# Optimization experiments

Hardware: AMD Instinct MI355X
Metric: run time of the kernel (lower is better)

The kernel has to match this reference:

```python
import jax, jax.numpy as jnp
import numpy as np

# Canonical topology: root object with K arrays, each array has L number leaves.
# Weights are tied across paths (tie_weights_containers=tie_weights_primitives=True),
# NumberEmbedder runs in eval mode with initial buffers mean=0, sqmean=1 -> identity norm.

K, L, D = 8192, 128, 64


def setup_inputs() -> dict:
    key = jax.random.key(0)
    ks = jax.random.split(key, 16)
    s = 1.0 / np.sqrt(D)
    return {
        "x": jax.random.normal(ks[0], (K, L), dtype=jnp.float32),
        "W_num": jax.random.normal(ks[1], (D, 1), dtype=jnp.float32) * s,
        "b_num": jax.random.normal(ks[2], (D,), dtype=jnp.float32) * s,
        "W_ih": jax.random.normal(ks[3], (4 * D, 2 * D), dtype=jnp.float32) * s,
        "W_hh": jax.random.normal(ks[4], (4 * D, D), dtype=jnp.float32) * s,
        "b_ih": jax.random.normal(ks[5], (4 * D,), dtype=jnp.float32) * s,
        "b_hh": jax.random.normal(ks[6], (4 * D,), dtype=jnp.float32) * s,
        "W_aout": jax.random.normal(ks[7], (D, D), dtype=jnp.float32) * s,
        "b_aout": jax.random.normal(ks[8], (D,), dtype=jnp.float32) * s,
        "W_fh": jax.random.normal(ks[9], (D, D), dtype=jnp.float32) * s,
        "b_fh": jax.random.normal(ks[10], (D,), dtype=jnp.float32) * s,
        "W_iouh": jax.random.normal(ks[11], (3 * D, D), dtype=jnp.float32) * s,
        "b_iouh": jax.random.normal(ks[12], (3 * D,), dtype=jnp.float32) * s,
        "W_oout": jax.random.normal(ks[13], (D, D), dtype=jnp.float32) * s,
        "b_oout": jax.random.normal(ks[14], (D,), dtype=jnp.float32) * s,
    }


def _forward(x, W_num, b_num, W_ih, W_hh, b_ih, b_hh, W_aout, b_aout,
             W_fh, b_fh, W_iouh, b_iouh, W_oout, b_oout):
    d = W_hh.shape[1]
    # --- NumberEmbedder: Linear(1, d) on identity-normalized numbers; c = 0 ---
    emb = x[..., None] * W_num[:, 0] + b_num          # [K, L, d]
    xs = jnp.transpose(emb, (1, 0, 2))                # [L, K, d] time-major for scan
    # --- ArrayEmbedder: LSTMCell over children; input = cat(child_h, child_c) ---
    # child_c is identically zero, so only the first half of W_ih contributes.
    W_ih_h = W_ih[:, :d]                              # [4d, d]
    bias = b_ih + b_hh                                # [4d]

    def step(carry, x_t):
        h, c = carry
        gates = x_t @ W_ih_h.T + h @ W_hh.T + bias    # [K, 4d]
        i, f, g, o = jnp.split(gates, 4, axis=1)
        c2 = jax.nn.sigmoid(f) * c + jax.nn.sigmoid(i) * jnp.tanh(g)
        h2 = jax.nn.sigmoid(o) * jnp.tanh(c2)
        return (h2, c2), None

    h0 = jnp.zeros((x.shape[0], d), dtype=x.dtype)
    (h_arr, c_arr), _ = jax.lax.scan(step, (h0, h0), xs)
    h_hat = h_arr @ W_aout.T + b_aout                 # [K, d] array lout
    # --- ObjectEmbedder: child-sum TreeLSTM over the K array states ---
    f = h_hat @ W_fh.T + b_fh                         # [K, d]
    fc_sum = jnp.sum(jax.nn.sigmoid(f) * c_arr, axis=0, keepdims=True)  # [1, d]
    hs_bar = jnp.sum(h_hat, axis=0, keepdims=True)    # [1, d]
    iou = hs_bar @ W_iouh.T + b_iouh                  # [1, 3d]
    i, o, u = jnp.split(iou, 3, axis=1)
    c_obj = jax.nn.sigmoid(i) * jnp.tanh(u) + fc_sum
    h_obj = jax.nn.sigmoid(o) * jnp.tanh(c_obj)
    h_hat_obj = h_obj @ W_oout.T + b_oout             # [1, d] object lout
    # root forward returns cat(h, c)
    return jnp.concatenate([h_hat_obj, c_obj], axis=1)  # [1, 2d]


def reference(x, W_num, b_num, W_ih, W_hh, b_ih, b_hh, W_aout, b_aout,
              W_fh, b_fh, W_iouh, b_iouh, W_oout, b_oout):
    return _forward(x, W_num, b_num, W_ih, W_hh, b_ih, b_hh, W_aout, b_aout,
                    W_fh, b_fh, W_iouh, b_iouh, W_oout, b_oout)
```

## Files before the change

kernel.cpp:

```cpp
#include <hip/hip_runtime.h>
#include <cstddef>

#define D   64
#define L   128
#define NT  256
#define ROWS 16
#define XSS 132
#define HBS 72
#define NBLK 512
#define LOG2E 1.4426950408889634f

typedef __attribute__((ext_vector_type(8))) short short8;
typedef __attribute__((ext_vector_type(4))) float floatx4;
typedef __attribute__((ext_vector_type(2))) float f2;

__device__ __forceinline__ float fast_rcp(float x) {
#if defined(__has_builtin)
#if __has_builtin(__builtin_amdgcn_rcpf)
  return __builtin_amdgcn_rcpf(x);
#else
  return 1.0f / x;
#endif
#else
  return 1.0f / x;
#endif
}
__device__ __forceinline__ float ex2(float x) {
#if defined(__has_builtin)
#if __has_builtin(__builtin_amdgcn_exp2f)
  return __builtin_amdgcn_exp2f(x);
#else
  return __builtin_exp2f(x);
#endif
#else
  return __builtin_exp2f(x);
#endif
}
__device__ __forceinline__ f2 ex2_2(f2 v) { return (f2){ex2(v.x), ex2(v.y)}; }
__device__ __forceinline__ f2 rcp_2(f2 v) { return (f2){fast_rcp(v.x), fast_rcp(v.y)}; }
__device__ __forceinline__ float sig_plain(float x) {
  return fast_rcp(1.0f + ex2(-LOG2E * x));
}
__device__ __forceinline__ float tanh2(float G) {
  return fmaf(2.0f, fast_rcp(1.0f + ex2(G)), -1.0f);
}
__device__ __forceinline__ unsigned short f2bf_rtne(float f) {
  unsigned int u = __float_as_uint(f);
  u += 0x7fffu + ((u >> 16) & 1u);
  return (unsigned short)(u >> 16);
}
__device__ __forceinline__ float bf2f(unsigned short s) {
  return __uint_as_float(((unsigned int)s) << 16);
}

__global__ __launch_bounds__(NT, 2)
void lstm_main(const float* __restrict__ x,
               const float* __restrict__ W_num,
               const float* __restrict__ b_num,
               const float* __restrict__ W_ih,
               const float* __restrict__ W_hh,
               const float* __restrict__ b_ih,
               const float* __restrict__ b_hh,
               const float* __restrict__ W_aout,
               const float* __restrict__ b_aout,
               const float* __restrict__ W_fh,
               const float* __restrict__ b_fh,
               const float* __restrict__ W_iouh,
               const float* __restrict__ b_iouh,
               const float* __restrict__ W_oout,
               const float* __restrict__ b_oout,
               float* __restrict__ acc_out,
               float* __restrict__ out)
{
  __shared__ __align__(16) float xs[ROWS * XSS];
  __shared__ __align__(16) short hb[2][ROWS * HBS];
  __shared__ float sacc[2 * D];
  __shared__ float hobj[D];
  __shared__ int   is_last;

  const int tid  = threadIdx.x;
  const int w    = tid >> 6;
  const int lane = tid & 63;
  const int quad = lane >> 4;
  const int c16  = lane & 15;
  const int k0   = blockIdx.x * ROWS;
  const int dcol = w * 16 + c16;

  for (int i = tid; i < ROWS * (L / 4); i += NT) {
    int r = i >> 5, c4 = i & 31;
    float4 v = ((const float4*)(x + (size_t)(k0 + r) * L))[c4];
    float* dst = &xs[r * XSS + c4 * 4];
    dst[0] = v.x; dst[1] = v.y; dst[2] = v.z; dst[3] = v.w;
  }
  for (int i = tid; i < ROWS * HBS; i += NT) hb[0][i] = 0;

  const float gscale[4] = {-LOG2E, -LOG2E, -2.0f * LOG2E, -LOG2E};

  float An[4], Bc[4];
#pragma unroll
  for (int g = 0; g < 4; ++g) {
    int j = g * 64 + dcol;
    const float4* wr = (const float4*)(W_ih + (size_t)j * (2 * D));
    float a = 0.0f, b = b_ih[j] + b_hh[j];
#pragma unroll
    for (int e4 = 0; e4 < 16; ++e4) {
      float4 wv = wr[e4];
      float4 wn = ((const float4*)W_num)[e4];
      float4 bn = ((const float4*)b_num)[e4];
      a = fmaf(wn.x, wv.x, a); a = fmaf(wn.y, wv.y, a);
      a = fmaf(wn.z, wv.z, a); a = fmaf(wn.w, wv.w, a);
      b = fmaf(bn.x, wv.x, b); b = fmaf(bn.y, wv.y, b);
      b = fmaf(bn.z, wv.z, b); b = fmaf(bn.w, wv.w, b);
    }
    An[g] = a * gscale[g]; Bc[g] = b * gscale[g];
  }

  short8 Bf[4][2];
#pragma unroll
  for (int g = 0; g < 4; ++g) {
#pragma unroll
    for (int kk = 0; kk < 2; ++kk) {
      const float4* wp = (const float4*)(W_hh + (size_t)(g * 64 + dcol) * D
                                         + kk * 32 + quad * 8);
      float wv[8];
      float4 w0 = wp[0], w1 = wp[1];
      wv[0]=w0.x; wv[1]=w0.y; wv[2]=w0.z; wv[3]=w0.w;
      wv[4]=w1.x; wv[5]=w1.y; wv[6]=w1.z; wv[7]=w1.w;
      short8 hi8;
#pragma unroll
      for (int j = 0; j < 8; ++j)
        hi8[j] = (short)f2bf_rtne(wv[j] * gscale[g]);
      Bf[g][kk] = hi8;
    }
  }

  const f2 one2  = {1.0f, 1.0f};
  const f2 m2l2  = {-2.0f * LOG2E, -2.0f * LOG2E};
  f2 creg2[2] = {{0.f, 0.f}, {0.f, 0.f}};
  f2 hreg2[2] = {{0.f, 0.f}, {0.f, 0.f}};
  __syncthreads();

  int p = 0;
  for (int t4 = 0; t4 < L; t4 += 4) {
    float4 xq[4];
#pragma unroll
    for (int r = 0; r < 4; ++r)
      xq[r] = *(const float4*)&xs[(quad * 4 + r) * XSS + t4];
#pragma unroll
    for (int u = 0; u < 4; ++u) {
      short8 ahi[2];
#pragma unroll
      for (int kk = 0; kk < 2; ++kk)
        ahi[kk] = *(const short8*)&hb[p][c16 * HBS + kk * 32 + quad * 8];
      f2 xv01 = {xq[0][u], xq[1][u]};
      f2 xv23 = {xq[2][u], xq[3][u]};
      floatx4 acc[4];
#pragma unroll
      for (int g = 0; g < 4; ++g) {
        f2 A2 = {An[g], An[g]}, B2 = {Bc[g], Bc[g]};
        f2 i01 = A2 * xv01 + B2;
        f2 i23 = A2 * xv23 + B2;
        acc[g] = (floatx4){i01.x, i01.y, i23.x, i23.y};
      }
#pragma unroll
      for (int kk = 0; kk < 2; ++kk) {
#pragma unroll
        for (int g = 0; g < 4; ++g)
          acc[g] = __builtin_amdgcn_mfma_f32_16x16x32_bf16(ahi[kk], Bf[g][kk], acc[g], 0, 0, 0);
      }
#pragma unroll
      for (int h = 0; h < 2; ++h) {
        f2 Gi = {acc[0][2*h], acc[0][2*h+1]};
        f2 Gf = {acc[1][2*h], acc[1][2*h+1]};
        f2 Gg = {acc[2][2*h], acc[2][2*h+1]};
        f2 Go = {acc[3][2*h], acc[3][2*h+1]};
        f2 Ei = ex2_2(Gi), Ef = ex2_2(Gf), Eg = ex2_2(Gg), Eo = ex2_2(Go);
        f2 pf = Ef + one2, pi = Ei + one2, pg = Eg + one2, mg = one2 - Eg;
        f2 pig = pi * pg;
        f2 num = creg2[h] * pig + mg * pf;
        f2 c2  = num * rcp_2(pf * pig);
        creg2[h] = c2;
        f2 Ec = ex2_2(c2 * m2l2);
        f2 po = Eo + one2, pc = Ec + one2, mc = one2 - Ec;
        f2 h2 = mc * rcp_2(po * pc);
        hreg2[h] = h2;
        int row0 = quad * 4 + 2 * h;
        hb[p ^ 1][row0 * HBS + dcol]       = (short)f2bf_rtne(h2.x);
        hb[p ^ 1][(row0 + 1) * HBS + dcol] = (short)f2bf_rtne(h2.y);
      }
      __syncthreads();
      p ^= 1;
    }
  }

  float creg[4] = {creg2[0].x, creg2[0].y, creg2[1].x, creg2[1].y};
  float hreg[4] = {hreg2[0].x, hreg2[0].y, hreg2[1].x, hreg2[1].y};

#pragma unroll
  for (int r = 0; r < 4; ++r) xs[(quad * 4 + r) * XSS + dcol] = hreg[r];
  __syncthreads();

  float hhat[4];
#pragma unroll
  for (int r = 0; r < 4; ++r) {
    float a = b_aout[dcol];
    const float4* wa = (const float4*)(W_aout + (size_t)dcol * D);
    const float* hp = &xs[(quad * 4 + r) * XSS];
#pragma unroll
    for (int e4 = 0; e4 < 16; ++e4) {
      float4 wv = wa[e4];
      a = fmaf(wv.x, hp[e4*4+0], a); a = fmaf(wv.y, hp[e4*4+1], a);
      a = fmaf(wv.z, hp[e4*4+2], a); a = fmaf(wv.w, hp[e4*4+3], a);
    }
    hhat[r] = a;
  }
  __syncthreads();
#pragma unroll
  for (int r = 0; r < 4; ++r) xs[(quad * 4 + r) * XSS + 64 + dcol] = hhat[r];
  __syncthreads();

  float pfc = 0.0f, phs = 0.0f;
#pragma unroll
  for (int r = 0; r < 4; ++r) {
    float f = b_fh[dcol];
    const float4* wf = (const float4*)(W_fh + (size_t)dcol * D);
    const float* hp = &xs[(quad * 4 + r) * XSS + 64];
#pragma unroll
    for (int e4 = 0; e4 < 16; ++e4) {
      float4 wv = wf[e4];
      f = fmaf(wv.x, hp[e4*4+0], f); f = fmaf(wv.y, hp[e4*4+1], f);
      f = fmaf(wv.z, hp[e4*4+2], f); f = fmaf(wv.w, hp[e4*4+3], f);
    }
    pfc = fmaf(sig_plain(f), creg[r], pfc);
    phs += hhat[r];
  }
  pfc += __shfl_xor(pfc, 16); pfc += __shfl_xor(pfc, 32);
  phs += __shfl_xor(phs, 16); phs += __shfl_xor(phs, 32);
  if (quad == 0) {
    atomicAdd(acc_out + dcol, pfc);
    atomicAdd(acc_out + D + dcol, phs);
  }

  __threadfence();
  if (tid == 0) {
    unsigned int prev = __hip_atomic_fetch_add((unsigned int*)(acc_out + 2 * D), 1u,
                                               __ATOMIC_ACQ_REL, __HIP_MEMORY_SCOPE_AGENT);
    is_last = (prev == NBLK - 1) ? 1 : 0;
  }
  __syncthreads();
  if (!is_last) return;
  __threadfence();
  if (tid < 2 * D)
    sacc[tid] = __hip_atomic_load(acc_out + tid, __ATOMIC_RELAXED, __HIP_MEMORY_SCOPE_AGENT);
  __syncthreads();
  if (tid < D) {
    const int d = tid;
    float vi = b_iouh[d], vo = b_iouh[D + d], vu = b_iouh[2 * D + d];
    for (int e = 0; e < D; ++e) {
      float hs = sacc[D + e];
      vi = fmaf(W_iouh[(size_t)d * D + e],           hs, vi);
      vo = fmaf(W_iouh[(size_t)(D + d) * D + e],     hs, vo);
      vu = fmaf(W_iouh[(size_t)(2 * D + d) * D + e], hs, vu);
    }
    float c_obj = sig_plain(vi) * tanh2(-2.0f * LOG2E * vu) + sacc[d];
    float h_obj = sig_plain(vo) * tanh2(-2.0f * LOG2E * c_obj);
    hobj[d] = h_obj;
    out[D + d] = c_obj;
  }
  __syncthreads();
  if (tid < D) {
    const int d = tid;
    float hh = b_oout[d];
    for (int e = 0; e < D; ++e) hh = fmaf(W_oout[(size_t)d * D + e], hobj[e], hh);
    out[d] = hh;
  }
}

extern "C" void kernel_launch(void* const* d_in, const int* in_sizes, int n_in,
                              void* d_out, int out_size, void* d_ws, size_t ws_size,
                              hipStream_t stream) {
  const float* x      = (const float*)d_in[0];
  const float* W_num  = (const float*)d_in[1];
  const float* b_num  = (const float*)d_in[2];
  const float* W_ih   = (const float*)d_in[3];
  const float* W_hh   = (const float*)d_in[4];
  const float* b_ih   = (const float*)d_in[5];
  const float* b_hh   = (const float*)d_in[6];
  const float* W_aout = (const float*)d_in[7];
  const float* b_aout = (const float*)d_in[8];
  const float* W_fh   = (const float*)d_in[9];
  const float* b_fh   = (const float*)d_in[10];
  const float* W_iouh = (const float*)d_in[11];
  const float* b_iouh = (const float*)d_in[12];
  const float* W_oout = (const float*)d_in[13];
  const float* b_oout = (const float*)d_in[14];
  float* acc = (float*)d_ws;
  float* out = (float*)d_out;

  hipMemsetAsync(d_ws, 0, (2 * D + 1) * sizeof(float), stream);
  lstm_main<<<NBLK, NT, 0, stream>>>(x, W_num, b_num, W_ih, W_hh, b_ih, b_hh,
                                     W_aout, b_aout, W_fh, b_fh,
                                     W_iouh, b_iouh, W_oout, b_oout, acc, out);
}
```

Baseline: 202.3 us.

## Split LSTM gate nonlinearity across twice as many waves per block

The block grows from 4 to 8 waves. Each pair of waves redundantly computes the same MFMA gate tiles, and each wave then handles only half of the accumulator rows for the sigmoid/tanh cell update. The epilogue projections are split the same way. The aim is to shorten the per-timestep serial elementwise chain in the latency-bound recurrence and to give the CU more waves for hiding latency. The cost is doubled MFMA work and more register pressure under the tighter launch bound.

```diff
diff --git a/kernel.cpp b/kernel.cpp
--- a/kernel.cpp
+++ b/kernel.cpp
@@ -3,7 +3,7 @@
 
 #define D   64
 #define L   128
-#define NT  256
+#define NT  512
 #define ROWS 16
 #define XSS 132
 #define HBS 72
@@ -49,11 +49,8 @@
   u += 0x7fffu + ((u >> 16) & 1u);
   return (unsigned short)(u >> 16);
 }
-__device__ __forceinline__ float bf2f(unsigned short s) {
-  return __uint_as_float(((unsigned int)s) << 16);
-}
-
-__global__ __launch_bounds__(NT, 2)
+
+__global__ __launch_bounds__(NT, 4)
 void lstm_main(const float* __restrict__ x,
                const float* __restrict__ W_num,
                const float* __restrict__ b_num,
@@ -79,12 +76,14 @@
   __shared__ int   is_last;
 
   const int tid  = threadIdx.x;
-  const int w    = tid >> 6;
+  const int w8   = tid >> 6;
+  const int wlo  = w8 & 3;
+  const int whi  = w8 >> 2;
   const int lane = tid & 63;
   const int quad = lane >> 4;
   const int c16  = lane & 15;
   const int k0   = blockIdx.x * ROWS;
-  const int dcol = w * 16 + c16;
+  const int dcol = wlo * 16 + c16;
 
   for (int i = tid; i < ROWS * (L / 4); i += NT) {
     int r = i >> 5, c4 = i & 31;
@@ -136,8 +135,8 @@
 
   const f2 one2  = {1.0f, 1.0f};
   const f2 m2l2  = {-2.0f * LOG2E, -2.0f * LOG2E};
-  f2 creg2[2] = {{0.f, 0.f}, {0.f, 0.f}};
-  f2 hreg2[2] = {{0.f, 0.f}, {0.f, 0.f}};
+  f2 creg2 = {0.f, 0.f};
+  f2 hreg2 = {0.f, 0.f};
   __syncthreads();
 
   int p = 0;
@@ -168,8 +167,8 @@
         for (int g = 0; g < 4; ++g)
           acc[g] = __builtin_amdgcn_mfma_f32_16x16x32_bf16(ahi[kk], Bf[g][kk], acc[g], 0, 0, 0);
       }
-#pragma unroll
-      for (int h = 0; h < 2; ++h) {
+      {
+        const int h = whi;
         f2 Gi = {acc[0][2*h], acc[0][2*h+1]};
         f2 Gf = {acc[1][2*h], acc[1][2*h+1]};
         f2 Gg = {acc[2][2*h], acc[2][2*h+1]};
@@ -177,13 +176,13 @@
         f2 Ei = ex2_2(Gi), Ef = ex2_2(Gf), Eg = ex2_2(Gg), Eo = ex2_2(Go);
         f2 pf = Ef + one2, pi = Ei + one2, pg = Eg + one2, mg = one2 - Eg;
         f2 pig = pi * pg;
-        f2 num = creg2[h] * pig + mg * pf;
+        f2 num = creg2 * pig + mg * pf;
         f2 c2  = num * rcp_2(pf * pig);
-        creg2[h] = c2;
+        creg2 = c2;
         f2 Ec = ex2_2(c2 * m2l2);
         f2 po = Eo + one2, pc = Ec + one2, mc = one2 - Ec;
         f2 h2 = mc * rcp_2(po * pc);
-        hreg2[h] = h2;
+        hreg2 = h2;
         int row0 = quad * 4 + 2 * h;
         hb[p ^ 1][row0 * HBS + dcol]       = (short)f2bf_rtne(h2.x);
         hb[p ^ 1][(row0 + 1) * HBS + dcol] = (short)f2bf_rtne(h2.y);
@@ -193,19 +192,20 @@
     }
   }
 
-  float creg[4] = {creg2[0].x, creg2[0].y, creg2[1].x, creg2[1].y};
-  float hreg[4] = {hreg2[0].x, hreg2[0].y, hreg2[1].x, hreg2[1].y};
-
-#pragma unroll
-  for (int r = 0; r < 4; ++r) xs[(quad * 4 + r) * XSS + dcol] = hreg[r];
-  __syncthreads();
-
-  float hhat[4];
-#pragma unroll
-  for (int r = 0; r < 4; ++r) {
+  float creg[2] = {creg2.x, creg2.y};
+  float hreg[2] = {hreg2.x, hreg2.y};
+
+#pragma unroll
+  for (int r = 0; r < 2; ++r)
+    xs[(quad * 4 + 2 * whi + r) * XSS + dcol] = hreg[r];
+  __syncthreads();
+
+  float hhat[2];
+#pragma unroll
+  for (int r = 0; r < 2; ++r) {
     float a = b_aout[dcol];
     const float4* wa = (const float4*)(W_aout + (size_t)dcol * D);
-    const float* hp = &xs[(quad * 4 + r) * XSS];
+    const float* hp = &xs[(quad * 4 + 2 * whi + r) * XSS];
 #pragma unroll
     for (int e4 = 0; e4 < 16; ++e4) {
       float4 wv = wa[e4];
@@ -216,15 +216,16 @@
   }
   __syncthreads();
 #pragma unroll
-  for (int r = 0; r < 4; ++r) xs[(quad * 4 + r) * XSS + 64 + dcol] = hhat[r];
+  for (int r = 0; r < 2; ++r)
+    xs[(quad * 4 + 2 * whi + r) * XSS + 64 + dcol] = hhat[r];
   __syncthreads();
 
   float pfc = 0.0f, phs = 0.0f;
 #pragma unroll
-  for (int r = 0; r < 4; ++r) {
+  for (int r = 0; r < 2; ++r) {
     float f = b_fh[dcol];
     const float4* wf = (const float4*)(W_fh + (size_t)dcol * D);
-    const float* hp = &xs[(quad * 4 + r) * XSS + 64];
+    const float* hp = &xs[(quad * 4 + 2 * whi + r) * XSS + 64];
 #pragma unroll
     for (int e4 = 0; e4 < 16; ++e4) {
       float4 wv = wf[e4];
```

New measurement: 260.4 us. 1.29x slower.
